# Kernel optimization log

Hardware: AMD Instinct MI355X
Metric: run time of the kernel (lower is better)

Reference implementation:

```python
import jax, jax.numpy as jnp
import numpy as np

NUM_HEADS = 8
HEAD_DIM = 64  # hidden_dim // num_heads = 512 // 8
THRESHOLD = 0.5


def setup_inputs() -> dict:
    key = jax.random.key(0)
    ks = jax.random.split(key, 12)
    B, T, D, Hd = 4, 1024, 512, 512
    s = 0.02
    inp = {
        'x': jax.random.normal(ks[0], (B, T, D), dtype=jnp.float32),
        'Wq': jax.random.normal(ks[1], (D, Hd), dtype=jnp.float32) * s,
        'bq': jnp.zeros((Hd,), jnp.float32),
        'Wk': jax.random.normal(ks[2], (D, Hd), dtype=jnp.float32) * s,
        'bk': jnp.zeros((Hd,), jnp.float32),
        'Wv': jax.random.normal(ks[3], (D, Hd), dtype=jnp.float32) * s,
        'bv': jnp.zeros((Hd,), jnp.float32),
        'conv_w': jax.random.normal(ks[4], (NUM_HEADS,), dtype=jnp.float32) * 0.3,
        'conv_b': jnp.zeros((1,), jnp.float32),
        'Wfh': jax.random.normal(ks[5], (Hd, Hd), dtype=jnp.float32) * s,
        'bfh': jnp.zeros((Hd,), jnp.float32),
        'Wfg': jax.random.normal(ks[6], (Hd, Hd), dtype=jnp.float32) * s,
        'bfg': jnp.zeros((Hd,), jnp.float32),
        'Wrh': jax.random.normal(ks[7], (Hd, Hd), dtype=jnp.float32) * s,
        'brh': jnp.zeros((Hd,), jnp.float32),
        'Wrg': jax.random.normal(ks[8], (Hd, Hd), dtype=jnp.float32) * s,
        'brg': jnp.zeros((Hd,), jnp.float32),
    }
    return inp


def reference(x, Wq, bq, Wk, bk, Wv, bv, conv_w, conv_b,
              Wfh, bfh, Wfg, bfg, Wrh, brh, Wrg, brg):
    B, T, D = x.shape
    H, hd = NUM_HEADS, HEAD_DIM
    scale = hd ** -0.5

    q = (x @ Wq + bq).reshape(B, T, H, hd).transpose(0, 2, 1, 3)  # [B,H,T,hd]
    k = (x @ Wk + bk).reshape(B, T, H, hd).transpose(0, 2, 1, 3)
    v = (x @ Wv + bv).reshape(B, T, H, hd).transpose(0, 2, 1, 3)

    scores = jnp.einsum('bhqd,bhkd->bhqk', q, k) * scale        # [B,H,T,T]
    A_t = jax.nn.softmax(scores, axis=-1)

    # cross-head 1x1 conv: weighted sum over heads -> [B,1,T,T]
    R_f = jax.nn.sigmoid(jnp.einsum('bhqk,h->bqk', A_t, conv_w) + conv_b[0])
    R_f = R_f[:, None]                                           # [B,1,T,T]
    M_f = (R_f <= THRESHOLD).astype(A_t.dtype)
    M_r = (1.0 - R_f <= THRESHOLD).astype(A_t.dtype)

    A_f = jax.nn.softmax(A_t * M_f, axis=-1)
    A_r = jax.nn.softmax(A_t * M_r, axis=-1)

    T_f = jnp.einsum('bhqk,bhkd->bhqd', A_f, v).transpose(0, 2, 1, 3).reshape(B, T, H * hd)
    T_r = jnp.einsum('bhqk,bhkd->bhqd', A_r, v).transpose(0, 2, 1, 3).reshape(B, T, H * hd)

    F_f = T_f @ Wfh + bfh
    G_f = jax.nn.sigmoid(T_f @ Wfg + bfg)
    F_r = T_r @ Wrh + brh
    G_r = jax.nn.sigmoid(T_r @ Wrg + brg)

    G_cat = jax.nn.softmax(jnp.stack([G_f, G_r], axis=-1), axis=-1)  # [B,T,Hd,2]
    F_t = F_f * G_cat[..., 0] + F_r * G_cat[..., 1]
    return F_t
```

## Files before the change

### kernel.cpp

```cpp
#include <hip/hip_runtime.h>
#include <hip/hip_bf16.h>
#include <stdint.h>

typedef short bf16x8 __attribute__((ext_vector_type(8)));
typedef float f32x4 __attribute__((ext_vector_type(4)));

__device__ __forceinline__ unsigned short f2bf(float f) {
  union { float f; unsigned int u; } v;
  v.f = f;
  unsigned int u = v.u;
  u = (u + 0x7fffu + ((u >> 16) & 1u)) >> 16;
  return (unsigned short)u;
}

__device__ __forceinline__ unsigned int cvt_pk_bf16(float lo, float hi) {
  unsigned int r;
  asm("v_cvt_pk_bf16_f32 %0, %1, %2" : "=v"(r) : "v"(lo), "v"(hi));
  return r;
}

typedef union { bf16x8 v; unsigned int u[4]; } frag_u;

__device__ __forceinline__ void gload16(const void* g, void* lds) {
  __builtin_amdgcn_global_load_lds(
      (const __attribute__((address_space(1))) unsigned int*)(unsigned long long)g,
      (__attribute__((address_space(3))) unsigned int*)(unsigned long long)(unsigned)(unsigned long long)lds,
      16, 0, 0);
}

__device__ __forceinline__ bf16x8 lds_frag(const unsigned short* t, int row, int ch4q) {
  return *(const bf16x8*)(t + row * 64 + ((ch4q ^ (row & 7)) << 3));
}


__global__ __launch_bounds__(256) void prep_kernel(
    const float* __restrict__ x,
    const float* __restrict__ Wq, const float* __restrict__ Wk, const float* __restrict__ Wv,
    const float* __restrict__ Wfh, const float* __restrict__ Wfg,
    const float* __restrict__ Wrh, const float* __restrict__ Wrg,
    unsigned short* __restrict__ xb, unsigned short* __restrict__ wt) {
  int bid = blockIdx.x;
  int tid = threadIdx.x;
  if (bid < 256) {
    const float4* xi = (const float4*)x;
#pragma unroll
    for (int rep = 0; rep < 8; rep++) {
      int i = bid * 256 + tid + rep * 65536;
      float4 v = xi[i];
      uint2 u;
      u.x = cvt_pk_bf16(v.x, v.y);
      u.y = cvt_pk_bf16(v.z, v.w);
      *(uint2*)&xb[(size_t)i * 4] = u;
    }
  } else {
    __shared__ float tile[64][65];
    int t = bid - 256;
    int mat = t >> 6;
    t &= 63;
    int tr = (t >> 3) * 64, tc = (t & 7) * 64;
    const float* W = (mat == 0) ? Wq : (mat == 1) ? Wk : (mat == 2) ? Wv
                   : (mat == 3) ? Wfh : (mat == 4) ? Wfg : (mat == 5) ? Wrh : Wrg;
    unsigned short* Wt = wt + (size_t)mat * 512 * 512;
    for (int rep = 0; rep < 16; rep++) {
      int idx = rep * 256 + tid;
      int r = idx >> 6, c = idx & 63;
      tile[r][c] = W[(tr + r) * 512 + tc + c];
    }
    __syncthreads();
    for (int rep = 0; rep < 16; rep++) {
      int idx = rep * 256 + tid;
      int r = idx >> 6, c = idx & 63;
      Wt[(tc + r) * 512 + tr + c] = f2bf(tile[c][r]);
    }
  }
}

__global__ __launch_bounds__(256, 3) void qkv_kernel(
    const unsigned short* __restrict__ xb,
    const unsigned short* __restrict__ wtq, const unsigned short* __restrict__ wtk,
    const unsigned short* __restrict__ wtv,
    const float* __restrict__ bq, const float* __restrict__ bk, const float* __restrict__ bv,
    unsigned short* __restrict__ Qfrag, unsigned short* __restrict__ Kfrag,
    unsigned short* __restrict__ Vfrag) {
  __shared__ __attribute__((aligned(16))) unsigned short smem[16384];
  unsigned short* As = smem;
  unsigned short* Bq = smem + 4096;
  unsigned short* Bk = smem + 8192;
  unsigned short* Bv = smem + 12288;
  unsigned short* st0 = smem;
  unsigned short* st1 = smem + 4608;
  unsigned short* st2 = smem + 9216;
  const int m0 = blockIdx.y * 64, n0 = blockIdx.x * 64;
  const int tid = threadIdx.x, w = tid >> 6, lane = tid & 63;
  const int c = lane & 15, quad = lane >> 4;
  const int wm = w & 1, wn = w >> 1;
  const int rsel = lane >> 3, csel = lane & 7;
  const int sc = csel ^ rsel;
  const char* Ag  = (const char*)xb  + (size_t)(m0 + w * 16 + rsel) * 1024 + sc * 16;
  const char* Bgq = (const char*)wtq + (size_t)(n0 + w * 16 + rsel) * 1024 + sc * 16;
  const char* Bgk = (const char*)wtk + (size_t)(n0 + w * 16 + rsel) * 1024 + sc * 16;
  const char* Bgv = (const char*)wtv + (size_t)(n0 + w * 16 + rsel) * 1024 + sc * 16;
  unsigned short* lA = &As[w * 1024];
  unsigned short* lQ = &Bq[w * 1024];
  unsigned short* lK = &Bk[w * 1024];
  unsigned short* lV = &Bv[w * 1024];

  f32x4 acc[3][2][2];
  f32x4 z4 = {0.f, 0.f, 0.f, 0.f};
#pragma unroll
  for (int o = 0; o < 3; o++)
#pragma unroll
    for (int i = 0; i < 2; i++)
#pragma unroll
      for (int j = 0; j < 2; j++) acc[o][i][j] = z4;

  for (int ks = 0; ks < 8; ks++) {
    if (ks) __syncthreads();
    const int kb = ks * 128;
    gload16(Ag + kb, lA);        gload16(Ag + kb + 8192, lA + 512);
    gload16(Bgq + kb, lQ);       gload16(Bgq + kb + 8192, lQ + 512);
    gload16(Bgk + kb, lK);       gload16(Bgk + kb + 8192, lK + 512);
    gload16(Bgv + kb, lV);       gload16(Bgv + kb + 8192, lV + 512);
    __syncthreads();
#pragma unroll
    for (int ch = 0; ch < 2; ch++) {
      const int cq = ch * 4 + quad;
      bf16x8 a0 = lds_frag(As, wm * 32 + c, cq);
      bf16x8 a1 = lds_frag(As, wm * 32 + 16 + c, cq);
#pragma unroll
      for (int nt = 0; nt < 2; nt++) {
        const int rb = wn * 32 + nt * 16 + c;
        bf16x8 fq = lds_frag(Bq, rb, cq);
        bf16x8 fk = lds_frag(Bk, rb, cq);
        bf16x8 fv = lds_frag(Bv, rb, cq);
        acc[0][0][nt] = __builtin_amdgcn_mfma_f32_16x16x32_bf16(a0, fq, acc[0][0][nt], 0, 0, 0);
        acc[0][1][nt] = __builtin_amdgcn_mfma_f32_16x16x32_bf16(a1, fq, acc[0][1][nt], 0, 0, 0);
        acc[1][0][nt] = __builtin_amdgcn_mfma_f32_16x16x32_bf16(a0, fk, acc[1][0][nt], 0, 0, 0);
        acc[1][1][nt] = __builtin_amdgcn_mfma_f32_16x16x32_bf16(a1, fk, acc[1][1][nt], 0, 0, 0);
        acc[2][0][nt] = __builtin_amdgcn_mfma_f32_16x16x32_bf16(a0, fv, acc[2][0][nt], 0, 0, 0);
        acc[2][1][nt] = __builtin_amdgcn_mfma_f32_16x16x32_bf16(a1, fv, acc[2][1][nt], 0, 0, 0);
      }
    }
  }
  __syncthreads();

#pragma unroll
  for (int ms = 0; ms < 2; ms++)
#pragma unroll
    for (int nt = 0; nt < 2; nt++) {
      int n_l = wn * 32 + nt * 16 + c;
      int n = n0 + n_l;
      float biasq = bq[n], biask = bk[n], biasv = bv[n];
#pragma unroll
      for (int r = 0; r < 4; r++) {
        int m_l = wm * 32 + ms * 16 + quad * 4 + r;
        st0[m_l * 72 + n_l] = f2bf((acc[0][ms][nt][r] + biasq) * 0.125f);
        st1[m_l * 72 + n_l] = f2bf(acc[1][ms][nt][r] + biask);
        st2[n_l * 72 + m_l] = f2bf(acc[2][ms][nt][r] + biasv);
      }
    }
  __syncthreads();

  {
    const int h = n0 >> 6;
    const int bb = m0 >> 10, t0b = (m0 & 1023) >> 4;
#pragma unroll
    for (int sub = 0; sub < 2; sub++) {
      uint4 vq = *(uint4*)&st0[(w * 16 + c) * 72 + sub * 32 + quad * 8];
      uint4 vk = *(uint4*)&st1[(w * 16 + c) * 72 + sub * 32 + quad * 8];
      size_t base = (size_t)((bb * 64 + t0b + w) * 8192) + h * 1024 + sub * 512 + lane * 8;
      *(uint4*)&Qfrag[base] = vq;
      *(uint4*)&Kfrag[base] = vk;
    }
    const int ktq = t0b + w;
    const int ktp = ktq >> 1, half = ktq & 1;
#pragma unroll
    for (int dm = 0; dm < 4; dm++) {
      uint2 vv = *(uint2*)&st2[(dm * 16 + c) * 72 + w * 16 + quad * 4];
      size_t base = (size_t)(bb * 8 + h) * 65536 + (size_t)(ktp * 4 + dm) * 512
                  + lane * 8 + half * 4;
      *(uint2*)&Vfrag[base] = vv;
    }
  }
}

__global__ __launch_bounds__(512, 4) void zgate_kernel(
    const unsigned short* __restrict__ Qfrag, const unsigned short* __restrict__ Kfrag,
    const float* __restrict__ conv_w, const float* __restrict__ conv_b,
    unsigned int* __restrict__ Mfrag, float* __restrict__ Zinv) {
  const int b = blockIdx.x, qt = blockIdx.y;
  const int tid = threadIdx.x, w = tid >> 6, lane = tid & 63;
  const int c = lane & 15, quad = lane >> 4;
  __shared__ float zbuf[8][16];

  f32x4 z4 = {0.f, 0.f, 0.f, 0.f};
  const float cb = conv_b[0];
  const size_t qbase = (size_t)((b * 64 + qt) * 8192) + lane * 8;
  const int kt0 = w * 8;
  const size_t kb0 = (size_t)((b * 64 + kt0) * 8192) + lane * 8;

  f32x4 g[8];
#pragma unroll
  for (int j = 0; j < 8; j++) g[j] = {cb, cb, cb, cb};

  for (int h = 0; h < 8; h++) {
    bf16x8 qf0 = *(const bf16x8*)&Qfrag[qbase + h * 1024];
    bf16x8 qf1 = *(const bf16x8*)&Qfrag[qbase + h * 1024 + 512];
    f32x4 p[8];
    float zh = 0.f;
#pragma unroll
    for (int j = 0; j < 8; j++) {
      const size_t kb = kb0 + (size_t)j * 8192 + h * 1024;
      bf16x8 kf0 = *(const bf16x8*)&Kfrag[kb];
      bf16x8 kf1 = *(const bf16x8*)&Kfrag[kb + 512];
      f32x4 s = __builtin_amdgcn_mfma_f32_16x16x32_bf16(kf0, qf0, z4, 0, 0, 0);
      s = __builtin_amdgcn_mfma_f32_16x16x32_bf16(kf1, qf1, s, 0, 0, 0);
      p[j][0] = __expf(s[0]); p[j][1] = __expf(s[1]);
      p[j][2] = __expf(s[2]); p[j][3] = __expf(s[3]);
      zh += (p[j][0] + p[j][1]) + (p[j][2] + p[j][3]);
    }
    zh += __shfl_xor(zh, 16); zh += __shfl_xor(zh, 32);
    __syncthreads();
    if (quad == 0) zbuf[w][c] = zh;
    __syncthreads();
    float Z = ((zbuf[0][c] + zbuf[1][c]) + (zbuf[2][c] + zbuf[3][c]))
            + ((zbuf[4][c] + zbuf[5][c]) + (zbuf[6][c] + zbuf[7][c]));
    const float izq = 1.0f / Z;
    const float cwz = conv_w[h] * izq;
    if (w == 0 && quad == 0)
      Zinv[(size_t)((b * 64 + qt) * 8 + h) * 16 + c] = izq;
#pragma unroll
    for (int j = 0; j < 8; j++) {
      g[j][0] += cwz * p[j][0]; g[j][1] += cwz * p[j][1];
      g[j][2] += cwz * p[j][2]; g[j][3] += cwz * p[j][3];
    }
  }

#pragma unroll
  for (int j = 0; j < 4; j++) {
    unsigned int p0 = 0, p1 = 0;
#pragma unroll
    for (int r = 0; r < 4; r++) {
      p0 |= ((g[2 * j][r] <= 0.f ? 1u : 0u) | (g[2 * j][r] >= 0.f ? 2u : 0u)) << (8 * r);
      p1 |= ((g[2 * j + 1][r] <= 0.f ? 1u : 0u) | (g[2 * j + 1][r] >= 0.f ? 2u : 0u)) << (8 * r);
    }
    const int ktp = w * 4 + j;
    uint2 mm; mm.x = p0; mm.y = p1;
    *(uint2*)&Mfrag[(size_t)(b * 64 + qt) * 4096 + (size_t)ktp * 128 + lane * 2] = mm;
  }
}

__global__ __launch_bounds__(256, 4) void pv_kernel(
    const unsigned short* __restrict__ Qfrag, const unsigned short* __restrict__ Kfrag,
    const unsigned short* __restrict__ Vfrag,
    const unsigned int* __restrict__ Mfrag, const float* __restrict__ Zinv,
    unsigned short* __restrict__ Tfb, unsigned short* __restrict__ Trb) {
  const int h = blockIdx.x;
  const int b = blockIdx.y >> 5, qb = blockIdx.y & 31;
  const int tid = threadIdx.x, w = tid >> 6, lane = tid & 63;
  const int c = lane & 15, quad = lane >> 4;
  const int qloc = w & 1, kh = w >> 1;
  const int qt = qb * 2 + qloc;

  __shared__ __attribute__((aligned(16))) float red[2][4][256][4];
  __shared__ float zb[2][2][16];

  f32x4 z4 = {0.f, 0.f, 0.f, 0.f};
  const size_t qbase = (size_t)((b * 64 + qt) * 8192) + h * 1024 + lane * 8;
  bf16x8 qf0 = *(const bf16x8*)&Qfrag[qbase];
  bf16x8 qf1 = *(const bf16x8*)&Qfrag[qbase + 512];
  const float invZ = Zinv[(size_t)((b * 64 + qt) * 8 + h) * 16 + c];
  const size_t mbase = (size_t)(b * 64 + qt) * 4096 + lane * 2;
  const size_t vb0 = (size_t)(b * 8 + h) * 65536 + lane * 8;

  frag_u ones;
  ones.u[0] = 0x3F803F80u; ones.u[1] = 0x3F803F80u;
  ones.u[2] = 0x3F803F80u; ones.u[3] = 0x3F803F80u;

  f32x4 accf[4], accr[4];
#pragma unroll
  for (int i = 0; i < 4; i++) { accf[i] = z4; accr[i] = z4; }
  f32x4 acc_zf = z4, acc_zr = z4;

#pragma unroll 2
  for (int ip = 0; ip < 16; ip++) {
    const int ktp = kh * 16 + ip;
    const int kta = ktp * 2, ktb = kta + 1;
    const size_t kba = (size_t)((b * 64 + kta) * 8192) + h * 1024 + lane * 8;
    const size_t kbb = (size_t)((b * 64 + ktb) * 8192) + h * 1024 + lane * 8;
    bf16x8 ka0 = *(const bf16x8*)&Kfrag[kba];
    bf16x8 ka1 = *(const bf16x8*)&Kfrag[kba + 512];
    bf16x8 kb0 = *(const bf16x8*)&Kfrag[kbb];
    bf16x8 kb1 = *(const bf16x8*)&Kfrag[kbb + 512];
    f32x4 sa = __builtin_amdgcn_mfma_f32_16x16x32_bf16(ka0, qf0, z4, 0, 0, 0);
    sa = __builtin_amdgcn_mfma_f32_16x16x32_bf16(ka1, qf1, sa, 0, 0, 0);
    f32x4 sb = __builtin_amdgcn_mfma_f32_16x16x32_bf16(kb0, qf0, z4, 0, 0, 0);
    sb = __builtin_amdgcn_mfma_f32_16x16x32_bf16(kb1, qf1, sb, 0, 0, 0);
    const uint2 mp = *(const uint2*)&Mfrag[mbase + (size_t)ktp * 128];
    float ea[4], eb[4];
#pragma unroll
    for (int r = 0; r < 4; r++) {
      ea[r] = __expf(__expf(sa[r]) * invZ);
      eb[r] = __expf(__expf(sb[r]) * invZ);
    }
    frag_u pF, pR;
    {
      float f0 = (mp.x & 0x1u)        ? ea[0] : 1.f;
      float f1 = (mp.x & 0x100u)      ? ea[1] : 1.f;
      float f2 = (mp.x & 0x10000u)    ? ea[2] : 1.f;
      float f3 = (mp.x & 0x1000000u)  ? ea[3] : 1.f;
      float f4 = (mp.y & 0x1u)        ? eb[0] : 1.f;
      float f5 = (mp.y & 0x100u)      ? eb[1] : 1.f;
      float f6 = (mp.y & 0x10000u)    ? eb[2] : 1.f;
      float f7 = (mp.y & 0x1000000u)  ? eb[3] : 1.f;
      pF.u[0] = cvt_pk_bf16(f0, f1);
      pF.u[1] = cvt_pk_bf16(f2, f3);
      pF.u[2] = cvt_pk_bf16(f4, f5);
      pF.u[3] = cvt_pk_bf16(f6, f7);
      float r0 = (mp.x & 0x2u)        ? ea[0] : 1.f;
      float r1 = (mp.x & 0x200u)      ? ea[1] : 1.f;
      float r2 = (mp.x & 0x20000u)    ? ea[2] : 1.f;
      float r3 = (mp.x & 0x2000000u)  ? ea[3] : 1.f;
      float r4 = (mp.y & 0x2u)        ? eb[0] : 1.f;
      float r5 = (mp.y & 0x200u)      ? eb[1] : 1.f;
      float r6 = (mp.y & 0x20000u)    ? eb[2] : 1.f;
      float r7 = (mp.y & 0x2000000u)  ? eb[3] : 1.f;
      pR.u[0] = cvt_pk_bf16(r0, r1);
      pR.u[1] = cvt_pk_bf16(r2, r3);
      pR.u[2] = cvt_pk_bf16(r4, r5);
      pR.u[3] = cvt_pk_bf16(r6, r7);
    }
    acc_zf = __builtin_amdgcn_mfma_f32_16x16x32_bf16(ones.v, pF.v, acc_zf, 0, 0, 0);
    acc_zr = __builtin_amdgcn_mfma_f32_16x16x32_bf16(ones.v, pR.v, acc_zr, 0, 0, 0);
#pragma unroll
    for (int dm = 0; dm < 4; dm++) {
      bf16x8 vf = *(const bf16x8*)&Vfrag[vb0 + (size_t)(ktp * 4 + dm) * 512];
      accf[dm] = __builtin_amdgcn_mfma_f32_16x16x32_bf16(vf, pF.v, accf[dm], 0, 0, 0);
      accr[dm] = __builtin_amdgcn_mfma_f32_16x16x32_bf16(vf, pR.v, accr[dm], 0, 0, 0);
    }
  }

  if (kh == 1) {
#pragma unroll
    for (int dm = 0; dm < 4; dm++) *(f32x4*)red[qloc][dm][lane] = accf[dm];
    if (lane < 16) { zb[qloc][0][lane] = acc_zf[0]; zb[qloc][1][lane] = acc_zr[0]; }
  }
  __syncthreads();
  if (kh == 0) {
#pragma unroll
    for (int dm = 0; dm < 4; dm++) accf[dm] += *(f32x4*)red[qloc][dm][lane];
  }
  __syncthreads();
  if (kh == 1) {
#pragma unroll
    for (int dm = 0; dm < 4; dm++) *(f32x4*)red[qloc][dm][lane] = accr[dm];
  }
  __syncthreads();
  uint2 outf[4], outr[4];
  if (kh == 0) {
#pragma unroll
    for (int dm = 0; dm < 4; dm++) accr[dm] += *(f32x4*)red[qloc][dm][lane];
    const float zf = acc_zf[0] + zb[qloc][0][c];
    const float zr = acc_zr[0] + zb[qloc][1][c];
    const float izf = 1.0f / zf, izr = 1.0f / zr;
#pragma unroll
    for (int dm = 0; dm < 4; dm++) {
      outf[dm].x = cvt_pk_bf16(accf[dm][0] * izf, accf[dm][1] * izf);
      outf[dm].y = cvt_pk_bf16(accf[dm][2] * izf, accf[dm][3] * izf);
      outr[dm].x = cvt_pk_bf16(accr[dm][0] * izr, accr[dm][1] * izr);
      outr[dm].y = cvt_pk_bf16(accr[dm][2] * izr, accr[dm][3] * izr);
    }
  }
  __syncthreads();
  unsigned short* ts = (unsigned short*)red;
  if (kh == 0) {
    const int qrow = qloc * 16 + c;
#pragma unroll
    for (int dm = 0; dm < 4; dm++) {
      *(uint2*)&ts[qrow * 72 + dm * 16 + quad * 4] = outf[dm];
      *(uint2*)&ts[(32 + qrow) * 72 + dm * 16 + quad * 4] = outr[dm];
    }
  }
  __syncthreads();
  {
    const int row = tid >> 3, seg = tid & 7;
    const size_t g = (size_t)(b * 1024 + qb * 32 + row) * 512 + h * 64 + seg * 8;
    *(uint4*)&Tfb[g] = *(uint4*)&ts[row * 72 + seg * 8];
    *(uint4*)&Trb[g] = *(uint4*)&ts[(32 + row) * 72 + seg * 8];
  }
}

__global__ __launch_bounds__(256, 4) void final_kernel(
    const unsigned short* __restrict__ Tfb, const unsigned short* __restrict__ Trb,
    const unsigned short* __restrict__ wfh, const unsigned short* __restrict__ wfg,
    const unsigned short* __restrict__ wrh, const unsigned short* __restrict__ wrg,
    const float* __restrict__ bfh, const float* __restrict__ bfg,
    const float* __restrict__ brh, const float* __restrict__ brg,
    float* __restrict__ out) {
  __shared__ unsigned short Atf[32 * 64];
  __shared__ unsigned short Atr[32 * 64];
  __shared__ unsigned short Bfh[64 * 64];
  __shared__ unsigned short Bfg[64 * 64];
  __shared__ unsigned short Brh[64 * 64];
  __shared__ unsigned short Brg[64 * 64];
  const int m0 = blockIdx.y * 32, n0 = blockIdx.x * 64;
  const int tid = threadIdx.x, w = tid >> 6, lane = tid & 63;
  const int c = lane & 15, quad = lane >> 4;
  const int wm = w & 1, wn = w >> 1;
  const int rsel = lane >> 3, csel = lane & 7;
  const int sc = csel ^ rsel;
  const char* Agf = (const char*)Tfb + (size_t)(m0 + w * 8 + rsel) * 1024 + sc * 16;
  const char* Agr = (const char*)Trb + (size_t)(m0 + w * 8 + rsel) * 1024 + sc * 16;
  const char* Bg0 = (const char*)wfh + (size_t)(n0 + w * 16 + rsel) * 1024 + sc * 16;
  const char* Bg1 = (const char*)wfg + (size_t)(n0 + w * 16 + rsel) * 1024 + sc * 16;
  const char* Bg2 = (const char*)wrh + (size_t)(n0 + w * 16 + rsel) * 1024 + sc * 16;
  const char* Bg3 = (const char*)wrg + (size_t)(n0 + w * 16 + rsel) * 1024 + sc * 16;
  unsigned short* lAf = &Atf[w * 512];
  unsigned short* lAr = &Atr[w * 512];
  unsigned short* l0 = &Bfh[w * 1024];
  unsigned short* l1 = &Bfg[w * 1024];
  unsigned short* l2 = &Brh[w * 1024];
  unsigned short* l3 = &Brg[w * 1024];

  f32x4 acc[4][2];
  f32x4 z4 = {0.f, 0.f, 0.f, 0.f};
#pragma unroll
  for (int o = 0; o < 4; o++)
#pragma unroll
    for (int j = 0; j < 2; j++) acc[o][j] = z4;

  for (int ks = 0; ks < 8; ks++) {
    if (ks) __syncthreads();
    const int kb = ks * 128;
    gload16(Agf + kb, lAf);
    gload16(Agr + kb, lAr);
    gload16(Bg0 + kb, l0);   gload16(Bg0 + kb + 8192, l0 + 512);
    gload16(Bg1 + kb, l1);   gload16(Bg1 + kb + 8192, l1 + 512);
    gload16(Bg2 + kb, l2);   gload16(Bg2 + kb + 8192, l2 + 512);
    gload16(Bg3 + kb, l3);   gload16(Bg3 + kb + 8192, l3 + 512);
    __syncthreads();
#pragma unroll
    for (int ch = 0; ch < 2; ch++) {
      const int cq = ch * 4 + quad;
      bf16x8 af = lds_frag(Atf, wm * 16 + c, cq);
      bf16x8 ar = lds_frag(Atr, wm * 16 + c, cq);
#pragma unroll
      for (int nt = 0; nt < 2; nt++) {
        const int rb = wn * 32 + nt * 16 + c;
        bf16x8 f0 = lds_frag(Bfh, rb, cq);
        bf16x8 f1 = lds_frag(Bfg, rb, cq);
        bf16x8 f2 = lds_frag(Brh, rb, cq);
        bf16x8 f3 = lds_frag(Brg, rb, cq);
        acc[0][nt] = __builtin_amdgcn_mfma_f32_16x16x32_bf16(af, f0, acc[0][nt], 0, 0, 0);
        acc[1][nt] = __builtin_amdgcn_mfma_f32_16x16x32_bf16(af, f1, acc[1][nt], 0, 0, 0);
        acc[2][nt] = __builtin_amdgcn_mfma_f32_16x16x32_bf16(ar, f2, acc[2][nt], 0, 0, 0);
        acc[3][nt] = __builtin_amdgcn_mfma_f32_16x16x32_bf16(ar, f3, acc[3][nt], 0, 0, 0);
      }
    }
  }

#pragma unroll
  for (int nt = 0; nt < 2; nt++) {
    int n = n0 + wn * 32 + nt * 16 + c;
    float b0 = bfh[n], b1 = bfg[n], b2 = brh[n], b3 = brg[n];
    int t0 = m0 + wm * 16 + quad * 4;
#pragma unroll
    for (int r = 0; r < 4; r++) {
      int t = t0 + r;
      float Ff = acc[0][nt][r] + b0;
      float Gf = 1.0f / (1.0f + __expf(-(acc[1][nt][r] + b1)));
      float Fr = acc[2][nt][r] + b2;
      float Gr = 1.0f / (1.0f + __expf(-(acc[3][nt][r] + b3)));
      float ef = __expf(Gf), er = __expf(Gr);
      out[(size_t)t * 512 + n] = (Ff * ef + Fr * er) / (ef + er);
    }
  }
}

extern "C" void kernel_launch(void* const* d_in, const int* in_sizes, int n_in,
                              void* d_out, int out_size, void* d_ws, size_t ws_size,
                              hipStream_t stream) {
  const float* x   = (const float*)d_in[0];
  const float* Wq  = (const float*)d_in[1];
  const float* bq  = (const float*)d_in[2];
  const float* Wk  = (const float*)d_in[3];
  const float* bk  = (const float*)d_in[4];
  const float* Wv  = (const float*)d_in[5];
  const float* bv  = (const float*)d_in[6];
  const float* cw  = (const float*)d_in[7];
  const float* cb  = (const float*)d_in[8];
  const float* Wfh = (const float*)d_in[9];
  const float* bfh = (const float*)d_in[10];
  const float* Wfg = (const float*)d_in[11];
  const float* bfg = (const float*)d_in[12];
  const float* Wrh = (const float*)d_in[13];
  const float* brh = (const float*)d_in[14];
  const float* Wrg = (const float*)d_in[15];
  const float* brg = (const float*)d_in[16];

  char* ws = (char*)d_ws;
  const size_t MB = 1024 * 1024;
  unsigned short* xb    = (unsigned short*)(ws + 0 * MB);
  unsigned short* Qfrag = (unsigned short*)(ws + 4 * MB);
  unsigned short* Kfrag = (unsigned short*)(ws + 8 * MB);
  unsigned short* Vfrag = (unsigned short*)(ws + 12 * MB);
  unsigned short* Tfb   = (unsigned short*)(ws + 16 * MB);
  unsigned short* Trb   = (unsigned short*)(ws + 20 * MB);
  unsigned short* wt    = (unsigned short*)(ws + 24 * MB);
  unsigned int*   Mfrag = (unsigned int*)(ws + 28 * MB);
  float*          Zinv  = (float*)(ws + 32 * MB);
  const size_t WSZ = 512 * 512;

  prep_kernel<<<704, 256, 0, stream>>>(x, Wq, Wk, Wv, Wfh, Wfg, Wrh, Wrg, xb, wt);
  qkv_kernel<<<dim3(8, 64), 256, 0, stream>>>(xb, wt + 0 * WSZ, wt + 1 * WSZ, wt + 2 * WSZ,
                                              bq, bk, bv, Qfrag, Kfrag, Vfrag);
  zgate_kernel<<<dim3(4, 64), 512, 0, stream>>>(Qfrag, Kfrag, cw, cb, Mfrag, Zinv);
  pv_kernel<<<dim3(8, 128), 256, 0, stream>>>(Qfrag, Kfrag, Vfrag, Mfrag, Zinv, Tfb, Trb);
  final_kernel<<<dim3(8, 128), 256, 0, stream>>>(Tfb, Trb, wt + 3 * WSZ, wt + 4 * WSZ,
                                                 wt + 5 * WSZ, wt + 6 * WSZ,
                                                 bfh, bfg, brh, brg, (float*)d_out);
}
```

Baseline: 178.3 us.

## Materialize normalized attention probabilities in zgate and reuse them in pv kernel

The zgate kernel now writes the normalized softmax probabilities A_t as bf16 fragments into a new workspace buffer instead of only the per-row inverse normalizer. The pv kernel reads these fragments directly instead of reloading K, recomputing QK^T with MFMAs and applying an extra exponential. This removes recompute and one transcendental per element, but adds a large write and read of the full B*H*T*T probability tensor through global memory and quantizes A_t to bf16 before the second softmax.

```diff
diff --git a/kernel.cpp b/kernel.cpp
--- a/kernel.cpp
+++ b/kernel.cpp
@@ -187,7 +187,7 @@
 __global__ __launch_bounds__(512, 4) void zgate_kernel(
     const unsigned short* __restrict__ Qfrag, const unsigned short* __restrict__ Kfrag,
     const float* __restrict__ conv_w, const float* __restrict__ conv_b,
-    unsigned int* __restrict__ Mfrag, float* __restrict__ Zinv) {
+    unsigned int* __restrict__ Mfrag, unsigned short* __restrict__ At) {
   const int b = blockIdx.x, qt = blockIdx.y;
   const int tid = threadIdx.x, w = tid >> 6, lane = tid & 63;
   const int c = lane & 15, quad = lane >> 4;
@@ -198,6 +198,7 @@
   const size_t qbase = (size_t)((b * 64 + qt) * 8192) + lane * 8;
   const int kt0 = w * 8;
   const size_t kb0 = (size_t)((b * 64 + kt0) * 8192) + lane * 8;
+  unsigned short* atp = At + (size_t)(b * 64 + qt) * 8 * 32 * 512 + lane * 8;
 
   f32x4 g[8];
 #pragma unroll
@@ -227,8 +228,16 @@
             + ((zbuf[4][c] + zbuf[5][c]) + (zbuf[6][c] + zbuf[7][c]));
     const float izq = 1.0f / Z;
     const float cwz = conv_w[h] * izq;
-    if (w == 0 && quad == 0)
-      Zinv[(size_t)((b * 64 + qt) * 8 + h) * 16 + c] = izq;
+    unsigned short* ath = atp + (size_t)h * 32 * 512;
+#pragma unroll
+    for (int j = 0; j < 4; j++) {
+      uint4 u;
+      u.x = cvt_pk_bf16(p[2 * j][0] * izq, p[2 * j][1] * izq);
+      u.y = cvt_pk_bf16(p[2 * j][2] * izq, p[2 * j][3] * izq);
+      u.z = cvt_pk_bf16(p[2 * j + 1][0] * izq, p[2 * j + 1][1] * izq);
+      u.w = cvt_pk_bf16(p[2 * j + 1][2] * izq, p[2 * j + 1][3] * izq);
+      *(uint4*)&ath[(size_t)(w * 4 + j) * 512] = u;
+    }
 #pragma unroll
     for (int j = 0; j < 8; j++) {
       g[j][0] += cwz * p[j][0]; g[j][1] += cwz * p[j][1];
@@ -251,9 +260,8 @@
 }
 
 __global__ __launch_bounds__(256, 4) void pv_kernel(
-    const unsigned short* __restrict__ Qfrag, const unsigned short* __restrict__ Kfrag,
-    const unsigned short* __restrict__ Vfrag,
-    const unsigned int* __restrict__ Mfrag, const float* __restrict__ Zinv,
+    const unsigned short* __restrict__ At, const unsigned short* __restrict__ Vfrag,
+    const unsigned int* __restrict__ Mfrag,
     unsigned short* __restrict__ Tfb, unsigned short* __restrict__ Trb) {
   const int h = blockIdx.x;
   const int b = blockIdx.y >> 5, qb = blockIdx.y & 31;
@@ -266,10 +274,7 @@
   __shared__ float zb[2][2][16];
 
   f32x4 z4 = {0.f, 0.f, 0.f, 0.f};
-  const size_t qbase = (size_t)((b * 64 + qt) * 8192) + h * 1024 + lane * 8;
-  bf16x8 qf0 = *(const bf16x8*)&Qfrag[qbase];
-  bf16x8 qf1 = *(const bf16x8*)&Qfrag[qbase + 512];
-  const float invZ = Zinv[(size_t)((b * 64 + qt) * 8 + h) * 16 + c];
+  const size_t abase = (size_t)((b * 64 + qt) * 8 + h) * 32 * 512 + lane * 8;
   const size_t mbase = (size_t)(b * 64 + qt) * 4096 + lane * 2;
   const size_t vb0 = (size_t)(b * 8 + h) * 65536 + lane * 8;
 
@@ -285,51 +290,27 @@
 #pragma unroll 2
   for (int ip = 0; ip < 16; ip++) {
     const int ktp = kh * 16 + ip;
-    const int kta = ktp * 2, ktb = kta + 1;
-    const size_t kba = (size_t)((b * 64 + kta) * 8192) + h * 1024 + lane * 8;
-    const size_t kbb = (size_t)((b * 64 + ktb) * 8192) + h * 1024 + lane * 8;
-    bf16x8 ka0 = *(const bf16x8*)&Kfrag[kba];
-    bf16x8 ka1 = *(const bf16x8*)&Kfrag[kba + 512];
-    bf16x8 kb0 = *(const bf16x8*)&Kfrag[kbb];
-    bf16x8 kb1 = *(const bf16x8*)&Kfrag[kbb + 512];
-    f32x4 sa = __builtin_amdgcn_mfma_f32_16x16x32_bf16(ka0, qf0, z4, 0, 0, 0);
-    sa = __builtin_amdgcn_mfma_f32_16x16x32_bf16(ka1, qf1, sa, 0, 0, 0);
-    f32x4 sb = __builtin_amdgcn_mfma_f32_16x16x32_bf16(kb0, qf0, z4, 0, 0, 0);
-    sb = __builtin_amdgcn_mfma_f32_16x16x32_bf16(kb1, qf1, sb, 0, 0, 0);
+    frag_u at;
+    *(uint4*)&at.u[0] = *(const uint4*)&At[abase + (size_t)ktp * 512];
     const uint2 mp = *(const uint2*)&Mfrag[mbase + (size_t)ktp * 128];
-    float ea[4], eb[4];
-#pragma unroll
-    for (int r = 0; r < 4; r++) {
-      ea[r] = __expf(__expf(sa[r]) * invZ);
-      eb[r] = __expf(__expf(sb[r]) * invZ);
+    float e[8];
+#pragma unroll
+    for (int i = 0; i < 4; i++) {
+      union { unsigned int u; float f; } lo, hi;
+      lo.u = at.u[i] << 16;
+      hi.u = at.u[i] & 0xffff0000u;
+      e[2 * i]     = __expf(lo.f);
+      e[2 * i + 1] = __expf(hi.f);
     }
     frag_u pF, pR;
-    {
-      float f0 = (mp.x & 0x1u)        ? ea[0] : 1.f;
-      float f1 = (mp.x & 0x100u)      ? ea[1] : 1.f;
-      float f2 = (mp.x & 0x10000u)    ? ea[2] : 1.f;
-      float f3 = (mp.x & 0x1000000u)  ? ea[3] : 1.f;
-      float f4 = (mp.y & 0x1u)        ? eb[0] : 1.f;
-      float f5 = (mp.y & 0x100u)      ? eb[1] : 1.f;
-      float f6 = (mp.y & 0x10000u)    ? eb[2] : 1.f;
-      float f7 = (mp.y & 0x1000000u)  ? eb[3] : 1.f;
-      pF.u[0] = cvt_pk_bf16(f0, f1);
-      pF.u[1] = cvt_pk_bf16(f2, f3);
-      pF.u[2] = cvt_pk_bf16(f4, f5);
-      pF.u[3] = cvt_pk_bf16(f6, f7);
-      float r0 = (mp.x & 0x2u)        ? ea[0] : 1.f;
-      float r1 = (mp.x & 0x200u)      ? ea[1] : 1.f;
-      float r2 = (mp.x & 0x20000u)    ? ea[2] : 1.f;
-      float r3 = (mp.x & 0x2000000u)  ? ea[3] : 1.f;
-      float r4 = (mp.y & 0x2u)        ? eb[0] : 1.f;
-      float r5 = (mp.y & 0x200u)      ? eb[1] : 1.f;
-      float r6 = (mp.y & 0x20000u)    ? eb[2] : 1.f;
-      float r7 = (mp.y & 0x2000000u)  ? eb[3] : 1.f;
-      pR.u[0] = cvt_pk_bf16(r0, r1);
-      pR.u[1] = cvt_pk_bf16(r2, r3);
-      pR.u[2] = cvt_pk_bf16(r4, r5);
-      pR.u[3] = cvt_pk_bf16(r6, r7);
-    }
+    pF.u[0] = cvt_pk_bf16((mp.x & 0x1u)       ? e[0] : 1.f, (mp.x & 0x100u)     ? e[1] : 1.f);
+    pF.u[1] = cvt_pk_bf16((mp.x & 0x10000u)   ? e[2] : 1.f, (mp.x & 0x1000000u) ? e[3] : 1.f);
+    pF.u[2] = cvt_pk_bf16((mp.y & 0x1u)       ? e[4] : 1.f, (mp.y & 0x100u)     ? e[5] : 1.f);
+    pF.u[3] = cvt_pk_bf16((mp.y & 0x10000u)   ? e[6] : 1.f, (mp.y & 0x1000000u) ? e[7] : 1.f);
+    pR.u[0] = cvt_pk_bf16((mp.x & 0x2u)       ? e[0] : 1.f, (mp.x & 0x200u)     ? e[1] : 1.f);
+    pR.u[1] = cvt_pk_bf16((mp.x & 0x20000u)   ? e[2] : 1.f, (mp.x & 0x2000000u) ? e[3] : 1.f);
+    pR.u[2] = cvt_pk_bf16((mp.y & 0x2u)       ? e[4] : 1.f, (mp.y & 0x200u)     ? e[5] : 1.f);
+    pR.u[3] = cvt_pk_bf16((mp.y & 0x20000u)   ? e[6] : 1.f, (mp.y & 0x2000000u) ? e[7] : 1.f);
     acc_zf = __builtin_amdgcn_mfma_f32_16x16x32_bf16(ones.v, pF.v, acc_zf, 0, 0, 0);
     acc_zr = __builtin_amdgcn_mfma_f32_16x16x32_bf16(ones.v, pR.v, acc_zr, 0, 0, 0);
 #pragma unroll
@@ -508,14 +489,14 @@
   unsigned short* Trb   = (unsigned short*)(ws + 20 * MB);
   unsigned short* wt    = (unsigned short*)(ws + 24 * MB);
   unsigned int*   Mfrag = (unsigned int*)(ws + 28 * MB);
-  float*          Zinv  = (float*)(ws + 32 * MB);
+  unsigned short* At    = (unsigned short*)(ws + 36 * MB);
   const size_t WSZ = 512 * 512;
 
   prep_kernel<<<704, 256, 0, stream>>>(x, Wq, Wk, Wv, Wfh, Wfg, Wrh, Wrg, xb, wt);
   qkv_kernel<<<dim3(8, 64), 256, 0, stream>>>(xb, wt + 0 * WSZ, wt + 1 * WSZ, wt + 2 * WSZ,
                                               bq, bk, bv, Qfrag, Kfrag, Vfrag);
-  zgate_kernel<<<dim3(4, 64), 512, 0, stream>>>(Qfrag, Kfrag, cw, cb, Mfrag, Zinv);
-  pv_kernel<<<dim3(8, 128), 256, 0, stream>>>(Qfrag, Kfrag, Vfrag, Mfrag, Zinv, Tfb, Trb);
+  zgate_kernel<<<dim3(4, 64), 512, 0, stream>>>(Qfrag, Kfrag, cw, cb, Mfrag, At);
+  pv_kernel<<<dim3(8, 128), 256, 0, stream>>>(At, Vfrag, Mfrag, Tfb, Trb);
   final_kernel<<<dim3(8, 128), 256, 0, stream>>>(Tfb, Trb, wt + 3 * WSZ, wt + 4 * WSZ,
                                                  wt + 5 * WSZ, wt + 6 * WSZ,
                                                  bfh, bfg, brh, brg, (float*)d_out);
```

Result: no change. 179.6 us (+0.7%).
